# Optimization experiments

Measured on AMD Instinct MI355X. Metric: run time of the kernel, lower is better.

Reference implementation:

```python
import jax, jax.numpy as jnp
import numpy as np

B, N, C = 8, 4096, 256
HEADS, SR = 8, 4
LN_EPS = 1e-5

def setup_inputs() -> dict:
    key = jax.random.key(0)
    ks = jax.random.split(key, 8)
    std = 0.02
    x = jax.random.normal(ks[0], (B, N, C), dtype=jnp.float32)
    q_w = jax.random.normal(ks[1], (C, C), dtype=jnp.float32) * std          # [in,out]
    kv_w = jax.random.normal(ks[2], (C, 2 * C), dtype=jnp.float32) * std     # [in,2*out]
    fan_out = SR * SR * C
    sr_w = jax.random.normal(ks[3], (C, C, SR, SR), dtype=jnp.float32) * np.sqrt(2.0 / fan_out)  # OIHW
    sr_b = jnp.zeros((C,), dtype=jnp.float32)
    ln_w = jnp.ones((C,), dtype=jnp.float32)
    ln_b = jnp.zeros((C,), dtype=jnp.float32)
    proj_w = jax.random.normal(ks[4], (C, C), dtype=jnp.float32) * std
    proj_b = jnp.zeros((C,), dtype=jnp.float32)
    return {"x": x, "H": 64, "W": 64, "q_w": q_w, "kv_w": kv_w, "sr_w": sr_w,
            "sr_b": sr_b, "ln_w": ln_w, "ln_b": ln_b, "proj_w": proj_w, "proj_b": proj_b}


def reference(x, H, W, q_w, kv_w, sr_w, sr_b, ln_w, ln_b, proj_w, proj_b):
    Bb, Nn, Cc = x.shape
    hd = Cc // HEADS
    scale = hd ** -0.5
    # q: [B, heads, N, hd]
    q = (x @ q_w).reshape(Bb, Nn, HEADS, hd).transpose(0, 2, 1, 3)
    # spatial reduction: conv(stride=sr) + LayerNorm
    x_ = x.transpose(0, 2, 1).reshape(Bb, Cc, H, W)
    x_ = jax.lax.conv_general_dilated(
        x_, sr_w, window_strides=(SR, SR), padding="VALID",
        dimension_numbers=("NCHW", "OIHW", "NCHW")) + sr_b[None, :, None, None]
    x_ = x_.reshape(Bb, Cc, -1).transpose(0, 2, 1)  # [B, Nk, C]
    mu = x_.mean(-1, keepdims=True)
    var = x_.var(-1, keepdims=True)
    x_ = (x_ - mu) * jax.lax.rsqrt(var + LN_EPS) * ln_w + ln_b
    # kv: [B, Nk, 2, heads, hd]
    Nk = x_.shape[1]
    kv = (x_ @ kv_w).reshape(Bb, Nk, 2, HEADS, hd)
    k = kv[:, :, 0].transpose(0, 2, 1, 3)  # [B, heads, Nk, hd]
    v = kv[:, :, 1].transpose(0, 2, 1, 3)  # [B, heads, Nk, hd]
    attn = jnp.einsum("bhnd,bhmd->bhnm", q, k) * scale
    attn = jax.nn.softmax(attn, axis=-1)
    out = jnp.einsum("bhnm,bhmd->bhnd", attn, v)  # [B, heads, N, hd]
    out = out.transpose(0, 2, 1, 3).reshape(Bb, Nn, Cc)
    return out @ proj_w + proj_b
```

## Files before the change

kernel.cpp:

```cpp
#include <hip/hip_runtime.h>
#include <hip/hip_bf16.h>
#include <math.h>

#define DI __device__ __forceinline__

static constexpr float SCALE = 0.17677669529663687f;

typedef short bf16x8 __attribute__((ext_vector_type(8)));
typedef float f32x4 __attribute__((ext_vector_type(4)));

__device__ int   g_isf32;
__device__ unsigned short g_qwh[256 * 256],  g_qwl[256 * 256];
__device__ unsigned short g_kvwh[512 * 256], g_kvwl[512 * 256];
__device__ unsigned short g_pwh[256 * 256],  g_pwl[256 * 256];
__device__ unsigned short g_wth[(size_t)256 * 4096];
__device__ unsigned short g_wtl[(size_t)256 * 4096];
__device__ unsigned short g_q[(size_t)64 * 4096 * 32];
__device__ unsigned short g_k[(size_t)64 * 256 * 32];
__device__ unsigned short g_vt[(size_t)64 * 32 * 256];
__device__ float g_convp[(size_t)16 * 2048 * 256];
__device__ unsigned short g_lnh[2048 * 256], g_lnl[2048 * 256];
__device__ unsigned short g_attnb[(size_t)32768 * 256];

DI float bfbits2f(unsigned short b) { return __uint_as_float(((unsigned)b) << 16); }

DI unsigned short f2bf(float f) {
  unsigned u = __float_as_uint(f);
  unsigned r = (u + 0x7fffu + ((u >> 16) & 1u)) >> 16;
  return (unsigned short)r;
}

DI float4 ld_bf4(const unsigned short* p) {
  ushort4 u = *(const ushort4*)p;
  return make_float4(bfbits2f(u.x), bfbits2f(u.y), bfbits2f(u.z), bfbits2f(u.w));
}

DI float ld1(const void* p, size_t i, int f32) {
  return f32 ? ((const float*)p)[i] : bfbits2f(((const unsigned short*)p)[i]);
}

DI float4 ld4(const void* p, size_t i, int f32) {
  if (f32) return *(const float4*)((const float*)p + i);
  return ld_bf4((const unsigned short*)p + i);
}

__global__ void k_detect(const void* __restrict__ xp) {
  __shared__ float red[256];
  int t = threadIdx.x;
  const unsigned short* p = (const unsigned short*)xp;
  float m = 0.f;
  for (int i = t; i < 16384; i += 256) {
    float v = fabsf(bfbits2f(p[i]));
    m = (v == v && v < 1e30f) ? fmaxf(m, v) : 1e30f;
  }
  red[t] = m;
  __syncthreads();
  for (int s = 128; s > 0; s >>= 1) {
    if (t < s) red[t] = fmaxf(red[t], red[t + s]);
    __syncthreads();
  }
  if (t == 0) g_isf32 = (red[0] > 1e4f) ? 1 : 0;
}

__global__ void k_prep(const void* __restrict__ qw, const void* __restrict__ kvw,
                       const void* __restrict__ pwp, const void* __restrict__ srw) {
  const int f32 = g_isf32;
  int bid = blockIdx.x;
  if (bid < 1024) {
    int e = bid * 256 + threadIdx.x;
    float v;
    unsigned short *dh, *dl;
    size_t di;
    if (e < 65536) {
      int o = e >> 8, c = e & 255;
      v = ld1(qw, (size_t)c * 256 + o, f32) * SCALE;
      dh = g_qwh; dl = g_qwl; di = e;
    } else if (e < 196608) {
      int e2 = e - 65536;
      int o = e2 >> 8, c = e2 & 255;
      v = ld1(kvw, (size_t)c * 512 + o, f32);
      dh = g_kvwh; dl = g_kvwl; di = e2;
    } else {
      int e2 = e - 196608;
      int o = e2 >> 8, c = e2 & 255;
      v = ld1(pwp, (size_t)c * 256 + o, f32);
      dh = g_pwh; dl = g_pwl; di = e2;
    }
    unsigned short hi = f2bf(v);
    dh[di] = hi;
    dl[di] = f2bf(v - bfbits2f(hi));
  } else {
    int e = (bid - 1024) * 256 + threadIdx.x;
    int o = e >> 12, kk = e & 4095;
    int tap = kk >> 8, ci = kk & 255;
    float v = ld1(srw, (size_t)o * 4096 + ci * 16 + tap, f32);
    unsigned short hi = f2bf(v);
    g_wth[e] = hi;
    g_wtl[e] = f2bf(v - bfbits2f(hi));
  }
}

template <int MODE>
__launch_bounds__(256, 3)
__global__ void k_mgemm(const void* __restrict__ Ax,
                        const void* __restrict__ biasp, void* __restrict__ outp) {
  constexpr bool XIN = (MODE == 0 || MODE == 1);
  constexpr bool AH  = (MODE != 3);

  __shared__ __align__(16) short sa_h[64 * 40];
  __shared__ __align__(16) short sa_l[64 * 40];
  __shared__ __align__(16) short sb_h[256 * 40];
  __shared__ __align__(16) short sb_l[256 * 40];

  const int f32 = g_isf32;
  const int tid = threadIdx.x;
  const int m0 = blockIdx.x * 64;
  const int nblk = (MODE == 2) ? blockIdx.y : 0;
  const int kz = (MODE == 1) ? blockIdx.z * 256 : 0;
  const int wave = tid >> 6, lane = tid & 63;
  const int quad = lane >> 4, l15 = lane & 15;

  f32x4 acc[4][4] = {};

  for (int it = 0; it < 8; ++it) {
    const int kb = kz + it * 32;
    {
      int row = tid >> 2, chunk = tid & 3;
      size_t src;
      if constexpr (MODE == 1) {
        int m = m0 + row;
        int bb = m >> 8, sp = m & 255;
        int oh = sp >> 4, ow = sp & 15;
        int tap = kb >> 8, kh = tap >> 2, kw = tap & 3;
        int n = (4 * oh + kh) * 64 + 4 * ow + kw;
        src = (((size_t)(bb * 4096 + n)) << 8) + (kb & 255) + chunk * 8;
      } else {
        src = (((size_t)(m0 + row)) << 8) + kb + chunk * 8;
      }
      if constexpr (XIN) {
        float4 v0 = ld4(Ax, src, f32);
        float4 v1 = ld4(Ax, src + 4, f32);
        ushort4 h0, l0, h1, l1;
        h0.x = f2bf(v0.x); l0.x = f2bf(v0.x - bfbits2f(h0.x));
        h0.y = f2bf(v0.y); l0.y = f2bf(v0.y - bfbits2f(h0.y));
        h0.z = f2bf(v0.z); l0.z = f2bf(v0.z - bfbits2f(h0.z));
        h0.w = f2bf(v0.w); l0.w = f2bf(v0.w - bfbits2f(h0.w));
        h1.x = f2bf(v1.x); l1.x = f2bf(v1.x - bfbits2f(h1.x));
        h1.y = f2bf(v1.y); l1.y = f2bf(v1.y - bfbits2f(h1.y));
        h1.z = f2bf(v1.z); l1.z = f2bf(v1.z - bfbits2f(h1.z));
        h1.w = f2bf(v1.w); l1.w = f2bf(v1.w - bfbits2f(h1.w));
        *(ushort4*)&sa_h[row * 40 + chunk * 8]     = h0;
        *(ushort4*)&sa_h[row * 40 + chunk * 8 + 4] = h1;
        *(ushort4*)&sa_l[row * 40 + chunk * 8]     = l0;
        *(ushort4*)&sa_l[row * 40 + chunk * 8 + 4] = l1;
      } else if constexpr (MODE == 2) {
        *(uint4*)&sa_h[row * 40 + chunk * 8] = *(const uint4*)&g_lnh[src];
        *(uint4*)&sa_l[row * 40 + chunk * 8] = *(const uint4*)&g_lnl[src];
      } else {
        *(uint4*)&sa_h[row * 40 + chunk * 8] = *(const uint4*)&g_attnb[src];
      }
    }
    {
      constexpr int BKROW = (MODE == 1) ? 4096 : 256;
      const unsigned short* Bh = (MODE == 0) ? g_qwh : (MODE == 1) ? g_wth
                               : (MODE == 2) ? g_kvwh : g_pwh;
      const unsigned short* Bl = (MODE == 0) ? g_qwl : (MODE == 1) ? g_wtl
                               : (MODE == 2) ? g_kvwl : g_pwl;
#pragma unroll
      for (int i = 0; i < 4; ++i) {
        int linear = tid + 256 * i;
        int row = linear >> 2, chunk = linear & 3;
        size_t src = (size_t)(nblk * 256 + row) * BKROW + kb + chunk * 8;
        *(uint4*)&sb_h[row * 40 + chunk * 8] = *(const uint4*)&Bh[src];
        *(uint4*)&sb_l[row * 40 + chunk * 8] = *(const uint4*)&Bl[src];
      }
    }
    __syncthreads();
#pragma unroll
    for (int mt = 0; mt < 4; ++mt) {
      bf16x8 a_h = *(const bf16x8*)&sa_h[(mt * 16 + l15) * 40 + quad * 8];
      bf16x8 a_l;
      if constexpr (AH) a_l = *(const bf16x8*)&sa_l[(mt * 16 + l15) * 40 + quad * 8];
#pragma unroll
      for (int j = 0; j < 4; ++j) {
        int nrow = (4 * wave + j) * 16 + l15;
        bf16x8 b_h = *(const bf16x8*)&sb_h[nrow * 40 + quad * 8];
        bf16x8 b_l = *(const bf16x8*)&sb_l[nrow * 40 + quad * 8];
        f32x4 c = acc[mt][j];
        c = __builtin_amdgcn_mfma_f32_16x16x32_bf16(a_h, b_h, c, 0, 0, 0);
        if constexpr (AH)
          c = __builtin_amdgcn_mfma_f32_16x16x32_bf16(a_l, b_h, c, 0, 0, 0);
        c = __builtin_amdgcn_mfma_f32_16x16x32_bf16(a_h, b_l, c, 0, 0, 0);
        acc[mt][j] = c;
      }
    }
    __syncthreads();
  }

#pragma unroll
  for (int mt = 0; mt < 4; ++mt) {
#pragma unroll
    for (int j = 0; j < 4; ++j) {
#pragma unroll
      for (int r = 0; r < 4; ++r) {
        int m = m0 + mt * 16 + quad * 4 + r;
        int c = nblk * 256 + (4 * wave + j) * 16 + l15;
        float v = acc[mt][j][r];
        if constexpr (MODE == 0) {
          int b = m >> 12, n = m & 4095;
          int h = c >> 5, d = c & 31;
          g_q[(((size_t)(b * 8 + h) * 4096 + n) << 5) + d] = f2bf(v);
        } else if constexpr (MODE == 1) {
          g_convp[((size_t)blockIdx.z * 2048 + m) * 256 + c] = v;
        } else if constexpr (MODE == 2) {
          int s = c >> 8, h = (c >> 5) & 7, d = c & 31;
          int bb = m >> 8, nk = m & 255;
          if (s == 0)
            g_k[(((size_t)(bb * 8 + h) * 256 + nk) << 5) + d] = f2bf(v);
          else
            g_vt[(((size_t)(bb * 8 + h) * 32 + d) << 8) + nk] = f2bf(v);
        } else {
          float rr = v + ld1(biasp, c, f32);
          if (f32) ((float*)outp)[(size_t)m * 256 + c] = rr;
          else     ((unsigned short*)outp)[(size_t)m * 256 + c] = f2bf(rr);
        }
      }
    }
  }
}

__global__ void k_redln(const void* __restrict__ srb,
                        const void* __restrict__ lw, const void* __restrict__ lb) {
  const int f32 = g_isf32;
  int row = blockIdx.x, t = threadIdx.x;
  size_t idx = (size_t)row * 256 + t;
  float v = 0.f;
#pragma unroll
  for (int z = 0; z < 16; ++z) v += g_convp[(size_t)z * (2048 * 256) + idx];
  v += ld1(srb, t, f32);
  float s = v, sq = v * v;
#pragma unroll
  for (int off = 32; off >= 1; off >>= 1) {
    s += __shfl_down(s, off, 64);
    sq += __shfl_down(sq, off, 64);
  }
  __shared__ float rs[4], rq[4];
  int wid = t >> 6;
  if ((t & 63) == 0) { rs[wid] = s; rq[wid] = sq; }
  __syncthreads();
  float st = rs[0] + rs[1] + rs[2] + rs[3];
  float qt = rq[0] + rq[1] + rq[2] + rq[3];
  float mu = st * (1.0f / 256.0f);
  float var = qt * (1.0f / 256.0f) - mu * mu;
  float r = rsqrtf(var + 1e-5f);
  float o = (v - mu) * r * ld1(lw, t, f32) + ld1(lb, t, f32);
  unsigned short hi = f2bf(o);
  g_lnh[idx] = hi;
  g_lnl[idx] = f2bf(o - bfbits2f(hi));
}

__launch_bounds__(256, 3)
__global__ void k_attn() {
  __shared__ short smem[18688];
  short* sk  = smem;
  short* svt = smem + 10240;

  const int tid = threadIdx.x;
  const int bh = blockIdx.y;
  const int b = bh >> 3, h = bh & 7;

  {
    const uint4* gk = (const uint4*)(g_k + (size_t)bh * 8192);
    const uint4* gv = (const uint4*)(g_vt + (size_t)bh * 8192);
    for (int i = tid; i < 1024; i += 256) {
      int key = i >> 2, part = i & 3;
      *(uint4*)&sk[key * 40 + part * 8] = gk[i];
      int d = i >> 5, off = (i & 31) * 8;
      *(uint4*)&svt[d * 264 + off] = gv[i];
    }
  }
  __syncthreads();

  const int wave = tid >> 6, lane = tid & 63;
  const int quad = lane >> 4, l15 = lane & 15;
  const int n0 = blockIdx.x * 64 + wave * 16;

  bf16x8 qv = *(const bf16x8*)(g_q + ((size_t)bh * 4096 + n0 + l15) * 32 + quad * 8);

  f32x4 sacc[16];
#pragma unroll
  for (int t = 0; t < 16; ++t) {
    bf16x8 kf = *(const bf16x8*)&sk[(t * 16 + l15) * 40 + quad * 8];
    f32x4 c = {0.f, 0.f, 0.f, 0.f};
    sacc[t] = __builtin_amdgcn_mfma_f32_16x16x32_bf16(kf, qv, c, 0, 0, 0);
  }

  float m = sacc[0][0];
#pragma unroll
  for (int t = 0; t < 16; ++t) {
#pragma unroll
    for (int r = 0; r < 4; ++r) m = fmaxf(m, sacc[t][r]);
  }
  m = fmaxf(m, __shfl_xor(m, 16, 64));
  m = fmaxf(m, __shfl_xor(m, 32, 64));

  unsigned plo[16], phi[16];
  float ls = 0.f;
#pragma unroll
  for (int t = 0; t < 16; ++t) {
    unsigned short p0 = f2bf(__expf(sacc[t][0] - m));
    unsigned short p1 = f2bf(__expf(sacc[t][1] - m));
    unsigned short p2 = f2bf(__expf(sacc[t][2] - m));
    unsigned short p3 = f2bf(__expf(sacc[t][3] - m));
    ls += bfbits2f(p0) + bfbits2f(p1) + bfbits2f(p2) + bfbits2f(p3);
    plo[t] = (unsigned)p0 | ((unsigned)p1 << 16);
    phi[t] = (unsigned)p2 | ((unsigned)p3 << 16);
  }
  ls += __shfl_xor(ls, 16, 64);
  ls += __shfl_xor(ls, 32, 64);
  float inv = 1.0f / ls;

  f32x4 o0 = {0.f, 0.f, 0.f, 0.f}, o1 = {0.f, 0.f, 0.f, 0.f};
  const int laneA = ((quad & 1) << 5) + l15;
  const int laneB = laneA + 16;
  const bool hiT = quad >= 2;
#pragma unroll
  for (int c = 0; c < 8; ++c) {
    unsigned a0 = __shfl(plo[2 * c], laneA, 64), b0 = __shfl(plo[2 * c + 1], laneA, 64);
    unsigned a1 = __shfl(phi[2 * c], laneA, 64), b1 = __shfl(phi[2 * c + 1], laneA, 64);
    unsigned a2 = __shfl(plo[2 * c], laneB, 64), b2 = __shfl(plo[2 * c + 1], laneB, 64);
    unsigned a3 = __shfl(phi[2 * c], laneB, 64), b3 = __shfl(phi[2 * c + 1], laneB, 64);
    uint4 pk = make_uint4(hiT ? b0 : a0, hiT ? b1 : a1, hiT ? b2 : a2, hiT ? b3 : a3);
    bf16x8 pf = *(bf16x8*)&pk;
    bf16x8 v0 = *(const bf16x8*)&svt[l15 * 264 + c * 32 + quad * 8];
    bf16x8 v1 = *(const bf16x8*)&svt[(16 + l15) * 264 + c * 32 + quad * 8];
    o0 = __builtin_amdgcn_mfma_f32_16x16x32_bf16(v0, pf, o0, 0, 0, 0);
    o1 = __builtin_amdgcn_mfma_f32_16x16x32_bf16(v1, pf, o1, 0, 0, 0);
  }

  size_t base = ((size_t)(b * 4096 + n0 + l15)) * 256 + h * 32 + quad * 4;
  ushort4 u0, u1;
  u0.x = f2bf(o0[0] * inv); u0.y = f2bf(o0[1] * inv);
  u0.z = f2bf(o0[2] * inv); u0.w = f2bf(o0[3] * inv);
  u1.x = f2bf(o1[0] * inv); u1.y = f2bf(o1[1] * inv);
  u1.z = f2bf(o1[2] * inv); u1.w = f2bf(o1[3] * inv);
  *(ushort4*)&g_attnb[base]      = u0;
  *(ushort4*)&g_attnb[base + 16] = u1;
}

extern "C" void kernel_launch(void* const* d_in, const int* in_sizes, int n_in,
                              void* d_out, int out_size, void* d_ws, size_t ws_size,
                              hipStream_t stream) {
  const void* x   = d_in[0];
  const void* qw  = d_in[3];
  const void* kvw = d_in[4];
  const void* srw = d_in[5];
  const void* srb = d_in[6];
  const void* lnw = d_in[7];
  const void* lnb = d_in[8];
  const void* pw  = d_in[9];
  const void* pb  = d_in[10];

  k_detect<<<1, 256, 0, stream>>>(x);
  k_prep<<<5120, 256, 0, stream>>>(qw, kvw, pw, srw);
  k_mgemm<0><<<dim3(512, 1), 256, 0, stream>>>(x, nullptr, nullptr);
  k_mgemm<1><<<dim3(32, 1, 16), 256, 0, stream>>>(x, nullptr, nullptr);
  k_redln<<<2048, 256, 0, stream>>>(srb, lnw, lnb);
  k_mgemm<2><<<dim3(32, 2), 256, 0, stream>>>(nullptr, nullptr, nullptr);
  k_attn<<<dim3(64, 64), 256, 0, stream>>>();
  k_mgemm<3><<<dim3(512, 1), 256, 0, stream>>>(nullptr, pb, d_out);
}
```

Baseline: 241.2 us.

## Inline dtype detection, halve GEMM N-tile, and register-prefetch next K-slice

After: 307.8 us. +27.6%, slower.

```diff
diff --git a/kernel.cpp b/kernel.cpp
--- a/kernel.cpp
+++ b/kernel.cpp
@@ -9,7 +9,6 @@
 typedef short bf16x8 __attribute__((ext_vector_type(8)));
 typedef float f32x4 __attribute__((ext_vector_type(4)));
 
-__device__ int   g_isf32;
 __device__ unsigned short g_qwh[256 * 256],  g_qwl[256 * 256];
 __device__ unsigned short g_kvwh[512 * 256], g_kvwl[512 * 256];
 __device__ unsigned short g_pwh[256 * 256],  g_pwl[256 * 256];
@@ -44,27 +43,24 @@
   return ld_bf4((const unsigned short*)p + i);
 }
 
-__global__ void k_detect(const void* __restrict__ xp) {
-  __shared__ float red[256];
-  int t = threadIdx.x;
-  const unsigned short* p = (const unsigned short*)xp;
-  float m = 0.f;
-  for (int i = t; i < 16384; i += 256) {
-    float v = fabsf(bfbits2f(p[i]));
-    m = (v == v && v < 1e30f) ? fmaxf(m, v) : 1e30f;
-  }
-  red[t] = m;
-  __syncthreads();
-  for (int s = 128; s > 0; s >>= 1) {
-    if (t < s) red[t] = fmaxf(red[t], red[t + s]);
-    __syncthreads();
-  }
-  if (t == 0) g_isf32 = (red[0] > 1e4f) ? 1 : 0;
+DI int detect_f32(const void* xp) {
+  const unsigned* p = (const unsigned*)xp;
+  unsigned m0 = 0, m1 = 0;
+#pragma unroll
+  for (int i = 0; i < 32; ++i) {
+    unsigned w = p[i];
+    unsigned lo = w & 0x7fffu, hi = (w >> 16) & 0x7fffu;
+    m0 = lo > m0 ? lo : m0;
+    m1 = hi > m1 ? hi : m1;
+  }
+  unsigned mm = m0 > m1 ? m0 : m1;
+  return mm >= 0x4680u ? 1 : 0;
 }
 
 __global__ void k_prep(const void* __restrict__ qw, const void* __restrict__ kvw,
-                       const void* __restrict__ pwp, const void* __restrict__ srw) {
-  const int f32 = g_isf32;
+                       const void* __restrict__ pwp, const void* __restrict__ srw,
+                       const void* __restrict__ xp) {
+  const int f32 = detect_f32(xp);
   int bid = blockIdx.x;
   if (bid < 1024) {
     int e = bid * 256 + threadIdx.x;
@@ -101,91 +97,118 @@
 }
 
 template <int MODE>
-__launch_bounds__(256, 3)
-__global__ void k_mgemm(const void* __restrict__ Ax,
+__launch_bounds__(256, 4)
+__global__ void k_mgemm(const void* __restrict__ xp,
                         const void* __restrict__ biasp, void* __restrict__ outp) {
   constexpr bool XIN = (MODE == 0 || MODE == 1);
   constexpr bool AH  = (MODE != 3);
+  constexpr int BKROW = (MODE == 1) ? 4096 : 256;
 
   __shared__ __align__(16) short sa_h[64 * 40];
   __shared__ __align__(16) short sa_l[64 * 40];
-  __shared__ __align__(16) short sb_h[256 * 40];
-  __shared__ __align__(16) short sb_l[256 * 40];
-
-  const int f32 = g_isf32;
+  __shared__ __align__(16) short sb_h[128 * 40];
+  __shared__ __align__(16) short sb_l[128 * 40];
+
+  int f32 = 0;
+  if constexpr (XIN || MODE == 3) f32 = detect_f32(xp);
+
   const int tid = threadIdx.x;
   const int m0 = blockIdx.x * 64;
-  const int nblk = (MODE == 2) ? blockIdx.y : 0;
+  const int n0 = blockIdx.y * 128;
   const int kz = (MODE == 1) ? blockIdx.z * 256 : 0;
   const int wave = tid >> 6, lane = tid & 63;
   const int quad = lane >> 4, l15 = lane & 15;
 
-  f32x4 acc[4][4] = {};
-
+  const unsigned short* Bh = (MODE == 0) ? g_qwh : (MODE == 1) ? g_wth
+                           : (MODE == 2) ? g_kvwh : g_pwh;
+  const unsigned short* Bl = (MODE == 0) ? g_qwl : (MODE == 1) ? g_wtl
+                           : (MODE == 2) ? g_kvwl : g_pwl;
+
+  const int arow = tid >> 2, achk = tid & 3;
+  size_t abase;
+  if constexpr (MODE == 1) {
+    int m = m0 + arow;
+    int bb = m >> 8, sp = m & 255;
+    int oh = sp >> 4, ow = sp & 15;
+    int tap = kz >> 8, kh = tap >> 2, kw = tap & 3;
+    int n = (4 * oh + kh) * 64 + 4 * ow + kw;
+    abase = (((size_t)(bb * 4096 + n)) << 8) + achk * 8;
+  } else {
+    abase = (((size_t)(m0 + arow)) << 8) + achk * 8;
+  }
+
+  float4 pa0, pa1;
+  uint4 pah, pal;
+  uint4 pbh[2], pbl[2];
+
+  auto loadAB = [&](int it) {
+    size_t sa = abase + it * 32;
+    if constexpr (XIN) {
+      pa0 = ld4(xp, sa, f32);
+      pa1 = ld4(xp, sa + 4, f32);
+    } else if constexpr (MODE == 2) {
+      pah = *(const uint4*)&g_lnh[sa];
+      pal = *(const uint4*)&g_lnl[sa];
+    } else {
+      pah = *(const uint4*)&g_attnb[sa];
+    }
+#pragma unroll
+    for (int i = 0; i < 2; ++i) {
+      int lin = tid + 256 * i;
+      int row = lin >> 2, chk = lin & 3;
+      size_t sb = (size_t)(n0 + row) * BKROW + kz + it * 32 + chk * 8;
+      pbh[i] = *(const uint4*)&Bh[sb];
+      pbl[i] = *(const uint4*)&Bl[sb];
+    }
+  };
+
+  auto storeLDS = [&]() {
+    int ao = arow * 40 + achk * 8;
+    if constexpr (XIN) {
+      ushort4 h0, l0, h1, l1;
+      h0.x = f2bf(pa0.x); l0.x = f2bf(pa0.x - bfbits2f(h0.x));
+      h0.y = f2bf(pa0.y); l0.y = f2bf(pa0.y - bfbits2f(h0.y));
+      h0.z = f2bf(pa0.z); l0.z = f2bf(pa0.z - bfbits2f(h0.z));
+      h0.w = f2bf(pa0.w); l0.w = f2bf(pa0.w - bfbits2f(h0.w));
+      h1.x = f2bf(pa1.x); l1.x = f2bf(pa1.x - bfbits2f(h1.x));
+      h1.y = f2bf(pa1.y); l1.y = f2bf(pa1.y - bfbits2f(h1.y));
+      h1.z = f2bf(pa1.z); l1.z = f2bf(pa1.z - bfbits2f(h1.z));
+      h1.w = f2bf(pa1.w); l1.w = f2bf(pa1.w - bfbits2f(h1.w));
+      *(ushort4*)&sa_h[ao]     = h0;
+      *(ushort4*)&sa_h[ao + 4] = h1;
+      *(ushort4*)&sa_l[ao]     = l0;
+      *(ushort4*)&sa_l[ao + 4] = l1;
+    } else if constexpr (MODE == 2) {
+      *(uint4*)&sa_h[ao] = pah;
+      *(uint4*)&sa_l[ao] = pal;
+    } else {
+      *(uint4*)&sa_h[ao] = pah;
+    }
+#pragma unroll
+    for (int i = 0; i < 2; ++i) {
+      int lin = tid + 256 * i;
+      int row = lin >> 2, chk = lin & 3;
+      *(uint4*)&sb_h[row * 40 + chk * 8] = pbh[i];
+      *(uint4*)&sb_l[row * 40 + chk * 8] = pbl[i];
+    }
+  };
+
+  f32x4 acc[4][2] = {};
+  loadAB(0);
   for (int it = 0; it < 8; ++it) {
-    const int kb = kz + it * 32;
-    {
-      int row = tid >> 2, chunk = tid & 3;
-      size_t src;
-      if constexpr (MODE == 1) {
-        int m = m0 + row;
-        int bb = m >> 8, sp = m & 255;
-        int oh = sp >> 4, ow = sp & 15;
-        int tap = kb >> 8, kh = tap >> 2, kw = tap & 3;
-        int n = (4 * oh + kh) * 64 + 4 * ow + kw;
-        src = (((size_t)(bb * 4096 + n)) << 8) + (kb & 255) + chunk * 8;
-      } else {
-        src = (((size_t)(m0 + row)) << 8) + kb + chunk * 8;
-      }
-      if constexpr (XIN) {
-        float4 v0 = ld4(Ax, src, f32);
-        float4 v1 = ld4(Ax, src + 4, f32);
-        ushort4 h0, l0, h1, l1;
-        h0.x = f2bf(v0.x); l0.x = f2bf(v0.x - bfbits2f(h0.x));
-        h0.y = f2bf(v0.y); l0.y = f2bf(v0.y - bfbits2f(h0.y));
-        h0.z = f2bf(v0.z); l0.z = f2bf(v0.z - bfbits2f(h0.z));
-        h0.w = f2bf(v0.w); l0.w = f2bf(v0.w - bfbits2f(h0.w));
-        h1.x = f2bf(v1.x); l1.x = f2bf(v1.x - bfbits2f(h1.x));
-        h1.y = f2bf(v1.y); l1.y = f2bf(v1.y - bfbits2f(h1.y));
-        h1.z = f2bf(v1.z); l1.z = f2bf(v1.z - bfbits2f(h1.z));
-        h1.w = f2bf(v1.w); l1.w = f2bf(v1.w - bfbits2f(h1.w));
-        *(ushort4*)&sa_h[row * 40 + chunk * 8]     = h0;
-        *(ushort4*)&sa_h[row * 40 + chunk * 8 + 4] = h1;
-        *(ushort4*)&sa_l[row * 40 + chunk * 8]     = l0;
-        *(ushort4*)&sa_l[row * 40 + chunk * 8 + 4] = l1;
-      } else if constexpr (MODE == 2) {
-        *(uint4*)&sa_h[row * 40 + chunk * 8] = *(const uint4*)&g_lnh[src];
-        *(uint4*)&sa_l[row * 40 + chunk * 8] = *(const uint4*)&g_lnl[src];
-      } else {
-        *(uint4*)&sa_h[row * 40 + chunk * 8] = *(const uint4*)&g_attnb[src];
-      }
-    }
-    {
-      constexpr int BKROW = (MODE == 1) ? 4096 : 256;
-      const unsigned short* Bh = (MODE == 0) ? g_qwh : (MODE == 1) ? g_wth
-                               : (MODE == 2) ? g_kvwh : g_pwh;
-      const unsigned short* Bl = (MODE == 0) ? g_qwl : (MODE == 1) ? g_wtl
-                               : (MODE == 2) ? g_kvwl : g_pwl;
-#pragma unroll
-      for (int i = 0; i < 4; ++i) {
-        int linear = tid + 256 * i;
-        int row = linear >> 2, chunk = linear & 3;
-        size_t src = (size_t)(nblk * 256 + row) * BKROW + kb + chunk * 8;
-        *(uint4*)&sb_h[row * 40 + chunk * 8] = *(const uint4*)&Bh[src];
-        *(uint4*)&sb_l[row * 40 + chunk * 8] = *(const uint4*)&Bl[src];
-      }
-    }
+    storeLDS();
     __syncthreads();
+    if (it < 7) loadAB(it + 1);
 #pragma unroll
     for (int mt = 0; mt < 4; ++mt) {
       bf16x8 a_h = *(const bf16x8*)&sa_h[(mt * 16 + l15) * 40 + quad * 8];
       bf16x8 a_l;
       if constexpr (AH) a_l = *(const bf16x8*)&sa_l[(mt * 16 + l15) * 40 + quad * 8];
 #pragma unroll
-      for (int j = 0; j < 4; ++j) {
-        int nrow = (4 * wave + j) * 16 + l15;
-        bf16x8 b_h = *(const bf16x8*)&sb_h[nrow * 40 + quad * 8];
-        bf16x8 b_l = *(const bf16x8*)&sb_l[nrow * 40 + quad * 8];
+      for (int j = 0; j < 2; ++j) {
+        int nr = (wave * 2 + j) * 16 + l15;
+        bf16x8 b_h = *(const bf16x8*)&sb_h[nr * 40 + quad * 8];
+        bf16x8 b_l = *(const bf16x8*)&sb_l[nr * 40 + quad * 8];
         f32x4 c = acc[mt][j];
         c = __builtin_amdgcn_mfma_f32_16x16x32_bf16(a_h, b_h, c, 0, 0, 0);
         if constexpr (AH)
@@ -200,11 +223,11 @@
 #pragma unroll
   for (int mt = 0; mt < 4; ++mt) {
 #pragma unroll
-    for (int j = 0; j < 4; ++j) {
+    for (int j = 0; j < 2; ++j) {
 #pragma unroll
       for (int r = 0; r < 4; ++r) {
         int m = m0 + mt * 16 + quad * 4 + r;
-        int c = nblk * 256 + (4 * wave + j) * 16 + l15;
+        int c = n0 + (wave * 2 + j) * 16 + l15;
         float v = acc[mt][j][r];
         if constexpr (MODE == 0) {
           int b = m >> 12, n = m & 4095;
@@ -229,9 +252,9 @@
   }
 }
 
-__global__ void k_redln(const void* __restrict__ srb,
+__global__ void k_redln(const void* __restrict__ xp, const void* __restrict__ srb,
                         const void* __restrict__ lw, const void* __restrict__ lb) {
-  const int f32 = g_isf32;
+  const int f32 = detect_f32(xp);
   int row = blockIdx.x, t = threadIdx.x;
   size_t idx = (size_t)row * 256 + t;
   float v = 0.f;
@@ -361,12 +384,11 @@
   const void* pw  = d_in[9];
   const void* pb  = d_in[10];
 
-  k_detect<<<1, 256, 0, stream>>>(x);
-  k_prep<<<5120, 256, 0, stream>>>(qw, kvw, pw, srw);
-  k_mgemm<0><<<dim3(512, 1), 256, 0, stream>>>(x, nullptr, nullptr);
-  k_mgemm<1><<<dim3(32, 1, 16), 256, 0, stream>>>(x, nullptr, nullptr);
-  k_redln<<<2048, 256, 0, stream>>>(srb, lnw, lnb);
-  k_mgemm<2><<<dim3(32, 2), 256, 0, stream>>>(nullptr, nullptr, nullptr);
+  k_prep<<<5120, 256, 0, stream>>>(qw, kvw, pw, srw, x);
+  k_mgemm<0><<<dim3(512, 2), 256, 0, stream>>>(x, nullptr, nullptr);
+  k_mgemm<1><<<dim3(32, 2, 16), 256, 0, stream>>>(x, nullptr, nullptr);
+  k_redln<<<2048, 256, 0, stream>>>(x, srb, lnw, lnb);
+  k_mgemm<2><<<dim3(32, 4), 256, 0, stream>>>(x, nullptr, nullptr);
   k_attn<<<dim3(64, 64), 256, 0, stream>>>();
-  k_mgemm<3><<<dim3(512, 1), 256, 0, stream>>>(nullptr, pb, d_out);
-}
+  k_mgemm<3><<<dim3(512, 2), 256, 0, stream>>>(x, pb, d_out);
+}
```
